# Kernel tuning notes

Measured on AMD Instinct MI355X. Metric: run time of the kernel, lower is better.

Reference implementation:

```python
import jax, jax.numpy as jnp
import numpy as np

T = 2_000_000  # timesteps


def setup_inputs() -> dict:
    key = jax.random.key(0)
    u = jax.random.normal(key, (T, 2), dtype=jnp.float32) * 10.0  # external forces per step
    x0 = jnp.zeros((4,), dtype=jnp.float32)  # [z1, v1, z2, v2]
    c = jnp.array([10.0, 10.0, 10.0], dtype=jnp.float32)   # trainable damping c1,c2,c3
    m = jnp.array([20.0, 10.0], dtype=jnp.float32)          # masses m1,m2 (frozen)
    k = jnp.array([2.0e3, 1.0e3, 5.0e3], dtype=jnp.float32) # stiffness k1,k2,k3 (frozen)
    dt = jnp.float32(0.002)
    return {"u": u, "x0": x0, "c": c, "m": m, "k": k, "dt": dt}


def reference(u, x0, c, m, k, dt):
    c1, c2, c3 = c[0], c[1], c[2]
    m1, m2 = m[0], m[1]
    k1, k2, k3 = k[0], k[1], k[2]

    def deriv(x, ut):
        # x = [z1, v1, z2, v2]; returns dx/dt = [v1, a1, v2, a2]
        z1, v1, z2, v2 = x[0], x[1], x[2], x[3]
        a1 = (ut[0] - (c1 + c2) * v1 + c2 * v2 - (k1 + k2) * z1 + k2 * z2) / m1
        a2 = (ut[1] - (c3 + c2) * v2 + c2 * v1 - (k3 + k2) * z2 + k2 * z1) / m2
        return jnp.stack([v1, a1, v2, a2])

    half = dt * 0.5

    def step(x, ut):
        s1 = deriv(x, ut)
        s2 = deriv(x + half * s1, ut)
        s3 = deriv(x + half * s2, ut)
        s4 = deriv(x + dt * s3, ut)
        xn = x + (dt / 6.0) * (s1 + 2.0 * s2 + 2.0 * s3 + s4)
        y = jnp.stack([xn[0], xn[2]])  # positions z1, z2 (matches cell output)
        return xn, y

    _, ys = jax.lax.scan(step, x0, u)
    return ys  # [T, 2]
```

## Files before the change

### kernel.cpp

```cpp
#include <hip/hip_runtime.h>

#define BLK 256
#define LS  16
#define SPB (BLK*LS)
#define STR (LS+1)

#define WS_M   0
#define WS_N   16
#define WS_SK  24
#define WS_GK  152
#define WS_AGG 304
#define WS_S1  2352

#define STEP4(Mx,Nx, s0,s1,s2,s3, ux,uy, n0,n1,n2,n3)                                              \
  n0 = fmaf(Mx[0],s0,  fmaf(Mx[1],s1,  fmaf(Mx[2],s2,  fmaf(Mx[3],s3,  fmaf(Nx[0],ux, Nx[1]*uy))))); \
  n1 = fmaf(Mx[4],s0,  fmaf(Mx[5],s1,  fmaf(Mx[6],s2,  fmaf(Mx[7],s3,  fmaf(Nx[2],ux, Nx[3]*uy))))); \
  n2 = fmaf(Mx[8],s0,  fmaf(Mx[9],s1,  fmaf(Mx[10],s2, fmaf(Mx[11],s3, fmaf(Nx[4],ux, Nx[5]*uy))))); \
  n3 = fmaf(Mx[12],s0, fmaf(Mx[13],s1, fmaf(Mx[14],s2, fmaf(Mx[15],s3, fmaf(Nx[6],ux, Nx[7]*uy)))));

__device__ __forceinline__ float4 aff_apply(const float* Mx, float4 l, float4 c) {
  float4 r;
  r.x = fmaf(Mx[0],l.x,  fmaf(Mx[1],l.y,  fmaf(Mx[2],l.z,  fmaf(Mx[3],l.w,  c.x))));
  r.y = fmaf(Mx[4],l.x,  fmaf(Mx[5],l.y,  fmaf(Mx[6],l.z,  fmaf(Mx[7],l.w,  c.y))));
  r.z = fmaf(Mx[8],l.x,  fmaf(Mx[9],l.y,  fmaf(Mx[10],l.z, fmaf(Mx[11],l.w, c.z))));
  r.w = fmaf(Mx[12],l.x, fmaf(Mx[13],l.y, fmaf(Mx[14],l.z, fmaf(Mx[15],l.w, c.w))));
  return r;
}

__device__ __forceinline__ float4 matvec(const float* Mx, float4 v) {
  return aff_apply(Mx, v, make_float4(0.f, 0.f, 0.f, 0.f));
}

__device__ __forceinline__ void mm4d(const double* X, const double* Y, double* Z) {
  for (int i = 0; i < 4; ++i)
    for (int j = 0; j < 4; ++j) {
      double s = 0.0;
      for (int l = 0; l < 4; ++l) s += X[i*4+l] * Y[l*4+j];
      Z[i*4+j] = s;
    }
}

__global__ void k_setup(const float* __restrict__ cin, const float* __restrict__ min_,
                        const float* __restrict__ kin, const float* __restrict__ dtin,
                        float* __restrict__ ws) {
  double c1 = cin[0], c2 = cin[1], c3 = cin[2];
  double m1 = min_[0], m2 = min_[1];
  double k1 = kin[0], k2 = kin[1], k3 = kin[2];
  double h  = dtin[0];

  double A[16] = { 0.0, 1.0, 0.0, 0.0,
                  -(k1+k2)/m1, -(c1+c2)/m1,  k2/m1,  c2/m1,
                   0.0, 0.0, 0.0, 1.0,
                   k2/m2,  c2/m2, -(k3+k2)/m2, -(c3+c2)/m2 };

  double Q[16], R[16], S[16], M[16], tmp[16];
  for (int i = 0; i < 16; ++i) Q[i] = ((i % 5 == 0) ? 1.0 : 0.0) + (h/4.0)*A[i];
  mm4d(A, Q, tmp);
  for (int i = 0; i < 16; ++i) R[i] = ((i % 5 == 0) ? 1.0 : 0.0) + (h/3.0)*tmp[i];
  mm4d(A, R, tmp);
  for (int i = 0; i < 16; ++i) S[i] = ((i % 5 == 0) ? 1.0 : 0.0) + (h/2.0)*tmp[i];
  mm4d(A, S, tmp);
  for (int i = 0; i < 16; ++i) M[i] = ((i % 5 == 0) ? 1.0 : 0.0) + h*tmp[i];

  double N[8];
  for (int i = 0; i < 4; ++i) {
    N[2*i+0] = h * S[i*4+1] / m1;
    N[2*i+1] = h * S[i*4+3] / m2;
  }

  for (int i = 0; i < 16; ++i) ws[WS_M+i] = (float)M[i];
  for (int i = 0; i < 8;  ++i) ws[WS_N+i] = (float)N[i];

  double P[16]; for (int i = 0; i < 16; ++i) P[i] = M[i];
  for (int r = 0; r < 4; ++r) { mm4d(P, P, tmp); for (int i = 0; i < 16; ++i) P[i] = tmp[i]; }

  for (int i = 0; i < 16; ++i) ws[WS_SK+i] = (float)P[i];
  for (int k = 1; k < 8; ++k) {
    mm4d(P, P, tmp); for (int i = 0; i < 16; ++i) P[i] = tmp[i];
    for (int i = 0; i < 16; ++i) ws[WS_SK+16*k+i] = (float)P[i];
  }
  mm4d(P, P, tmp); for (int i = 0; i < 16; ++i) P[i] = tmp[i];
  for (int i = 0; i < 16; ++i) ws[WS_GK+i] = (float)P[i];
  for (int k = 1; k < 9; ++k) {
    mm4d(P, P, tmp); for (int i = 0; i < 16; ++i) P[i] = tmp[i];
    for (int i = 0; i < 16; ++i) ws[WS_GK+16*k+i] = (float)P[i];
  }
}

__launch_bounds__(BLK)
__global__ void k_pass1(const float4* __restrict__ u4, const float* __restrict__ ws,
                        float4* __restrict__ s1out, float4* __restrict__ agg, int T2) {
  __shared__ float  uxp[BLK*STR];
  __shared__ float  uyp[BLK*STR];
  __shared__ float4 S1[BLK];
  __shared__ float  SKs[8*16];
  const int tid   = threadIdx.x;
  const int bid   = blockIdx.x;
  const int base2 = bid * SPB;

  float Mm[16], Nn[8];
  #pragma unroll
  for (int i = 0; i < 16; ++i) Mm[i] = ws[WS_M+i];
  #pragma unroll
  for (int i = 0; i < 8;  ++i) Nn[i] = ws[WS_N+i];
  if (tid < 128) SKs[tid] = ws[WS_SK + tid];

  #pragma unroll
  for (int kk = 0; kk < SPB/2/BLK; ++kk) {
    int idx4 = tid + kk*BLK;
    int s0 = 2*idx4;
    float4 v = make_float4(0.f, 0.f, 0.f, 0.f);
    if (base2 + s0 < T2) v = u4[(base2 >> 1) + idx4];
    int t0 = s0 >> 4, j0 = s0 & 15;
    int t1 = (s0+1) >> 4, j1 = (s0+1) & 15;
    uxp[t0*STR + j0] = v.x;  uyp[t0*STR + j0] = v.y;
    uxp[t1*STR + j1] = v.z;  uyp[t1*STR + j1] = v.w;
  }
  __syncthreads();

  float b0 = 0.f, b1 = 0.f, b2 = 0.f, b3 = 0.f;
  #pragma unroll
  for (int j = 0; j < LS; ++j) {
    float ux = uxp[tid*STR + j], uy = uyp[tid*STR + j];
    float n0, n1, n2, n3;
    STEP4(Mm, Nn, b0, b1, b2, b3, ux, uy, n0, n1, n2, n3);
    b0 = n0; b1 = n1; b2 = n2; b3 = n3;
  }
  S1[tid] = make_float4(b0, b1, b2, b3);
  __syncthreads();

  #pragma unroll
  for (int k = 0; k < 8; ++k) {
    int off = 1 << k;
    float4 l, c;
    bool act = (tid >= off);
    if (act) { l = S1[tid - off]; c = S1[tid]; }
    __syncthreads();
    if (act) S1[tid] = aff_apply(&SKs[16*k], l, c);
    __syncthreads();
  }

  s1out[bid * BLK + tid] = S1[tid];
  if (tid == BLK-1) agg[bid] = S1[BLK-1];
}

__launch_bounds__(BLK)
__global__ void k_pass3(const float4* __restrict__ u4, const float* __restrict__ ws,
                        const float4* __restrict__ s1buf, const float4* __restrict__ agg,
                        const float* __restrict__ x0in, float4* __restrict__ out4,
                        int T2, int nblk) {
  __shared__ float  uxp[BLK*STR];
  __shared__ float  uyp[BLK*STR];
  __shared__ float4 MA[512];
  __shared__ float4 MB[512];
  __shared__ float  SKs[8*16];
  __shared__ float  GKs[9*16];
  const int tid   = threadIdx.x;
  const int bid   = blockIdx.x;
  const int base2 = bid * SPB;

  float Mm[16], Nn[8];
  #pragma unroll
  for (int i = 0; i < 16; ++i) Mm[i] = ws[WS_M+i];
  #pragma unroll
  for (int i = 0; i < 8;  ++i) Nn[i] = ws[WS_N+i];
  if (tid < 128) SKs[tid] = ws[WS_SK + tid];
  if (tid < 144) GKs[tid] = ws[WS_GK + tid];

  #pragma unroll
  for (int kk = 0; kk < SPB/2/BLK; ++kk) {
    int idx4 = tid + kk*BLK;
    int s0 = 2*idx4;
    float4 v = make_float4(0.f, 0.f, 0.f, 0.f);
    if (base2 + s0 < T2) v = u4[(base2 >> 1) + idx4];
    int t0 = s0 >> 4, j0 = s0 & 15;
    int t1 = (s0+1) >> 4, j1 = (s0+1) & 15;
    uxp[t0*STR + j0] = v.x;  uyp[t0*STR + j0] = v.y;
    uxp[t1*STR + j1] = v.z;  uyp[t1*STR + j1] = v.w;
  }

  const int n = nblk + 1;
  #pragma unroll
  for (int j = 0; j < 2; ++j) {
    int i = tid + BLK*j;
    if (i < n) MA[i] = (i == 0) ? make_float4(x0in[0], x0in[1], x0in[2], x0in[3])
                                : agg[i-1];
  }
  __syncthreads();

  float4* Aa = MA; float4* Bb = MB;
  for (int k = 0; k < 9; ++k) {
    int off = 1 << k;
    if (off >= n) break;
    #pragma unroll
    for (int j = 0; j < 2; ++j) {
      int i = tid + BLK*j;
      if (i < n) {
        float4 v = Aa[i];
        if (i >= off) v = aff_apply(&GKs[16*k], Aa[i-off], v);
        Bb[i] = v;
      }
    }
    __syncthreads();
    float4* t = Aa; Aa = Bb; Bb = t;
  }

  float4 Xbs = Aa[bid];

  float4 v = Xbs;
  #pragma unroll
  for (int k = 0; k < 8; ++k)
    if (tid & (1 << k)) v = matvec(&SKs[16*k], v);
  float4 p = (tid > 0) ? s1buf[bid*BLK + tid - 1] : make_float4(0.f, 0.f, 0.f, 0.f);
  float x0 = v.x + p.x, x1 = v.y + p.y, x2 = v.z + p.z, x3 = v.w + p.w;

  #pragma unroll
  for (int j = 0; j < LS; ++j) {
    float ux = uxp[tid*STR + j], uy = uyp[tid*STR + j];
    float n0, n1, n2, n3;
    STEP4(Mm, Nn, x0, x1, x2, x3, ux, uy, n0, n1, n2, n3);
    x0 = n0; x1 = n1; x2 = n2; x3 = n3;
    uxp[tid*STR + j] = x0;
    uyp[tid*STR + j] = x2;
  }
  __syncthreads();

  #pragma unroll
  for (int kk = 0; kk < SPB/2/BLK; ++kk) {
    int idx4 = tid + kk*BLK;
    int s0 = 2*idx4;
    if (base2 + s0 < T2) {
      int t0 = s0 >> 4, j0 = s0 & 15;
      int t1 = (s0+1) >> 4, j1 = (s0+1) & 15;
      out4[(base2 >> 1) + idx4] = make_float4(uxp[t0*STR + j0], uyp[t0*STR + j0],
                                              uxp[t1*STR + j1], uyp[t1*STR + j1]);
    }
  }
}

extern "C" void kernel_launch(void* const* d_in, const int* in_sizes, int n_in,
                              void* d_out, int out_size, void* d_ws, size_t ws_size,
                              hipStream_t stream) {
  const float* u   = (const float*)d_in[0];
  const float* x0  = (const float*)d_in[1];
  const float* cc  = (const float*)d_in[2];
  const float* mm  = (const float*)d_in[3];
  const float* kk  = (const float*)d_in[4];
  const float* dt  = (const float*)d_in[5];

  const int T2   = in_sizes[0] / 2;
  const int nblk = (T2 + SPB - 1) / SPB;

  float*  ws   = (float*)d_ws;
  float4* agg  = (float4*)(ws + WS_AGG);
  float4* s1b  = (float4*)(ws + WS_S1);

  k_setup<<<1, 1, 0, stream>>>(cc, mm, kk, dt, ws);
  k_pass1<<<nblk, BLK, 0, stream>>>((const float4*)u, ws, s1b, agg, T2);
  k_pass3<<<nblk, BLK, 0, stream>>>((const float4*)u, ws, s1b, agg, x0,
                                    (float4*)d_out, T2, nblk);
}
```

Before: 98.51 us.

## Fuse serial setup kernel into pass kernels via wave-parallel shuffle matmuls

Removes the single-thread k_setup launch and instead has the first wavefront of every block in both passes compute the RK4 propagator, input matrix and power tables redundantly. It uses one lane per matrix element and __shfl in double precision. This eliminates a serial single-lane kernel and one launch on the critical path, along with the global-memory round trip for the coefficients. In exchange every block pays a few dozen shuffle-based double matmuls, though that work overlaps with its input loads.

```diff
diff --git a/kernel.cpp b/kernel.cpp
--- a/kernel.cpp
+++ b/kernel.cpp
@@ -5,12 +5,8 @@
 #define SPB (BLK*LS)
 #define STR (LS+1)
 
-#define WS_M   0
-#define WS_N   16
-#define WS_SK  24
-#define WS_GK  152
-#define WS_AGG 304
-#define WS_S1  2352
+#define WS_AGG 0
+#define WS_S1  2048
 
 #define STEP4(Mx,Nx, s0,s1,s2,s3, ux,uy, n0,n1,n2,n3)                                              \
   n0 = fmaf(Mx[0],s0,  fmaf(Mx[1],s1,  fmaf(Mx[2],s2,  fmaf(Mx[3],s3,  fmaf(Nx[0],ux, Nx[1]*uy))))); \
@@ -31,79 +27,85 @@
   return aff_apply(Mx, v, make_float4(0.f, 0.f, 0.f, 0.f));
 }
 
-__device__ __forceinline__ void mm4d(const double* X, const double* Y, double* Z) {
-  for (int i = 0; i < 4; ++i)
-    for (int j = 0; j < 4; ++j) {
-      double s = 0.0;
-      for (int l = 0; l < 4; ++l) s += X[i*4+l] * Y[l*4+j];
-      Z[i*4+j] = s;
-    }
-}
-
-__global__ void k_setup(const float* __restrict__ cin, const float* __restrict__ min_,
-                        const float* __restrict__ kin, const float* __restrict__ dtin,
-                        float* __restrict__ ws) {
+__device__ __forceinline__ double mm_el(double x, double y, int i, int j) {
+  double s = 0.0;
+  #pragma unroll
+  for (int l = 0; l < 4; ++l)
+    s = fma(__shfl(x, 4*i + l, 64), __shfl(y, 4*l + j, 64), s);
+  return s;
+}
+
+__device__ __forceinline__ void wave_setup(const float* __restrict__ cin,
+                                           const float* __restrict__ min_,
+                                           const float* __restrict__ kin,
+                                           const float* __restrict__ dtin,
+                                           float* Ms, float* Ns, float* SKs, float* GKs,
+                                           int lane, bool wantGK) {
   double c1 = cin[0], c2 = cin[1], c3 = cin[2];
   double m1 = min_[0], m2 = min_[1];
   double k1 = kin[0], k2 = kin[1], k3 = kin[2];
   double h  = dtin[0];
-
-  double A[16] = { 0.0, 1.0, 0.0, 0.0,
-                  -(k1+k2)/m1, -(c1+c2)/m1,  k2/m1,  c2/m1,
-                   0.0, 0.0, 0.0, 1.0,
-                   k2/m2,  c2/m2, -(k3+k2)/m2, -(c3+c2)/m2 };
-
-  double Q[16], R[16], S[16], M[16], tmp[16];
-  for (int i = 0; i < 16; ++i) Q[i] = ((i % 5 == 0) ? 1.0 : 0.0) + (h/4.0)*A[i];
-  mm4d(A, Q, tmp);
-  for (int i = 0; i < 16; ++i) R[i] = ((i % 5 == 0) ? 1.0 : 0.0) + (h/3.0)*tmp[i];
-  mm4d(A, R, tmp);
-  for (int i = 0; i < 16; ++i) S[i] = ((i % 5 == 0) ? 1.0 : 0.0) + (h/2.0)*tmp[i];
-  mm4d(A, S, tmp);
-  for (int i = 0; i < 16; ++i) M[i] = ((i % 5 == 0) ? 1.0 : 0.0) + h*tmp[i];
-
-  double N[8];
-  for (int i = 0; i < 4; ++i) {
-    N[2*i+0] = h * S[i*4+1] / m1;
-    N[2*i+1] = h * S[i*4+3] / m2;
-  }
-
-  for (int i = 0; i < 16; ++i) ws[WS_M+i] = (float)M[i];
-  for (int i = 0; i < 8;  ++i) ws[WS_N+i] = (float)N[i];
-
-  double P[16]; for (int i = 0; i < 16; ++i) P[i] = M[i];
-  for (int r = 0; r < 4; ++r) { mm4d(P, P, tmp); for (int i = 0; i < 16; ++i) P[i] = tmp[i]; }
-
-  for (int i = 0; i < 16; ++i) ws[WS_SK+i] = (float)P[i];
+  const int i = (lane >> 2) & 3, j = lane & 3;
+
+  double a;
+  if (i == 0)      a = (j == 1) ? 1.0 : 0.0;
+  else if (i == 2) a = (j == 3) ? 1.0 : 0.0;
+  else if (i == 1) a = (j==0) ? -(k1+k2)/m1 : (j==1) ? -(c1+c2)/m1
+                     : (j==2) ?  k2/m1      :  c2/m1;
+  else             a = (j==0) ?  k2/m2      : (j==1) ?  c2/m2
+                     : (j==2) ? -(k3+k2)/m2 : -(c3+c2)/m2;
+
+  const double id = (i == j) ? 1.0 : 0.0;
+  double q  = id + (h/4.0)*a;
+  double t  = mm_el(a, q,  i, j);
+  double r  = id + (h/3.0)*t;
+  t         = mm_el(a, r,  i, j);
+  double s_ = id + (h/2.0)*t;
+  t         = mm_el(a, s_, i, j);
+  double m  = id + h*t;
+  if (lane < 16) Ms[lane] = (float)m;
+
+  {
+    int e = lane & 7, ii = e >> 1, jp = e & 1, col = jp ? 3 : 1;
+    double sv = __shfl(s_, 4*ii + col, 64);
+    double nv = h * sv / (jp ? m2 : m1);
+    if (lane < 8) Ns[lane] = (float)nv;
+  }
+
+  double p = m;
+  #pragma unroll
+  for (int rr = 0; rr < 4; ++rr) p = mm_el(p, p, i, j);
+  if (lane < 16) SKs[lane] = (float)p;
+  #pragma unroll
   for (int k = 1; k < 8; ++k) {
-    mm4d(P, P, tmp); for (int i = 0; i < 16; ++i) P[i] = tmp[i];
-    for (int i = 0; i < 16; ++i) ws[WS_SK+16*k+i] = (float)P[i];
-  }
-  mm4d(P, P, tmp); for (int i = 0; i < 16; ++i) P[i] = tmp[i];
-  for (int i = 0; i < 16; ++i) ws[WS_GK+i] = (float)P[i];
-  for (int k = 1; k < 9; ++k) {
-    mm4d(P, P, tmp); for (int i = 0; i < 16; ++i) P[i] = tmp[i];
-    for (int i = 0; i < 16; ++i) ws[WS_GK+16*k+i] = (float)P[i];
+    p = mm_el(p, p, i, j);
+    if (lane < 16) SKs[16*k + lane] = (float)p;
+  }
+  if (wantGK) {
+    p = mm_el(p, p, i, j);
+    if (lane < 16) GKs[lane] = (float)p;
+    #pragma unroll
+    for (int k = 1; k < 9; ++k) {
+      p = mm_el(p, p, i, j);
+      if (lane < 16) GKs[16*k + lane] = (float)p;
+    }
   }
 }
 
 __launch_bounds__(BLK)
-__global__ void k_pass1(const float4* __restrict__ u4, const float* __restrict__ ws,
+__global__ void k_pass1(const float4* __restrict__ u4,
+                        const float* __restrict__ cc, const float* __restrict__ mmp,
+                        const float* __restrict__ kp, const float* __restrict__ dtp,
                         float4* __restrict__ s1out, float4* __restrict__ agg, int T2) {
   __shared__ float  uxp[BLK*STR];
   __shared__ float  uyp[BLK*STR];
   __shared__ float4 S1[BLK];
-  __shared__ float  SKs[8*16];
+  __shared__ float  Ms[16], Ns[8], SKs[8*16];
   const int tid   = threadIdx.x;
   const int bid   = blockIdx.x;
   const int base2 = bid * SPB;
 
-  float Mm[16], Nn[8];
-  #pragma unroll
-  for (int i = 0; i < 16; ++i) Mm[i] = ws[WS_M+i];
-  #pragma unroll
-  for (int i = 0; i < 8;  ++i) Nn[i] = ws[WS_N+i];
-  if (tid < 128) SKs[tid] = ws[WS_SK + tid];
+  if (tid < 64) wave_setup(cc, mmp, kp, dtp, Ms, Ns, SKs, nullptr, tid, false);
 
   #pragma unroll
   for (int kk = 0; kk < SPB/2/BLK; ++kk) {
@@ -118,6 +120,12 @@
   }
   __syncthreads();
 
+  float Mm[16], Nn[8];
+  #pragma unroll
+  for (int i = 0; i < 16; ++i) Mm[i] = Ms[i];
+  #pragma unroll
+  for (int i = 0; i < 8;  ++i) Nn[i] = Ns[i];
+
   float b0 = 0.f, b1 = 0.f, b2 = 0.f, b3 = 0.f;
   #pragma unroll
   for (int j = 0; j < LS; ++j) {
@@ -145,7 +153,9 @@
 }
 
 __launch_bounds__(BLK)
-__global__ void k_pass3(const float4* __restrict__ u4, const float* __restrict__ ws,
+__global__ void k_pass3(const float4* __restrict__ u4,
+                        const float* __restrict__ cc, const float* __restrict__ mmp,
+                        const float* __restrict__ kp, const float* __restrict__ dtp,
                         const float4* __restrict__ s1buf, const float4* __restrict__ agg,
                         const float* __restrict__ x0in, float4* __restrict__ out4,
                         int T2, int nblk) {
@@ -153,19 +163,12 @@
   __shared__ float  uyp[BLK*STR];
   __shared__ float4 MA[512];
   __shared__ float4 MB[512];
-  __shared__ float  SKs[8*16];
-  __shared__ float  GKs[9*16];
+  __shared__ float  Ms[16], Ns[8], SKs[8*16], GKs[9*16];
   const int tid   = threadIdx.x;
   const int bid   = blockIdx.x;
   const int base2 = bid * SPB;
 
-  float Mm[16], Nn[8];
-  #pragma unroll
-  for (int i = 0; i < 16; ++i) Mm[i] = ws[WS_M+i];
-  #pragma unroll
-  for (int i = 0; i < 8;  ++i) Nn[i] = ws[WS_N+i];
-  if (tid < 128) SKs[tid] = ws[WS_SK + tid];
-  if (tid < 144) GKs[tid] = ws[WS_GK + tid];
+  if (tid < 64) wave_setup(cc, mmp, kp, dtp, Ms, Ns, SKs, GKs, tid, true);
 
   #pragma unroll
   for (int kk = 0; kk < SPB/2/BLK; ++kk) {
@@ -187,6 +190,12 @@
                                 : agg[i-1];
   }
   __syncthreads();
+
+  float Mm[16], Nn[8];
+  #pragma unroll
+  for (int i = 0; i < 16; ++i) Mm[i] = Ms[i];
+  #pragma unroll
+  for (int i = 0; i < 8;  ++i) Nn[i] = Ns[i];
 
   float4* Aa = MA; float4* Bb = MB;
   for (int k = 0; k < 9; ++k) {
@@ -251,12 +260,11 @@
   const int T2   = in_sizes[0] / 2;
   const int nblk = (T2 + SPB - 1) / SPB;
 
-  float*  ws   = (float*)d_ws;
-  float4* agg  = (float4*)(ws + WS_AGG);
-  float4* s1b  = (float4*)(ws + WS_S1);
-
-  k_setup<<<1, 1, 0, stream>>>(cc, mm, kk, dt, ws);
-  k_pass1<<<nblk, BLK, 0, stream>>>((const float4*)u, ws, s1b, agg, T2);
-  k_pass3<<<nblk, BLK, 0, stream>>>((const float4*)u, ws, s1b, agg, x0,
+  float*  ws  = (float*)d_ws;
+  float4* agg = (float4*)(ws + WS_AGG);
+  float4* s1b = (float4*)(ws + WS_S1);
+
+  k_pass1<<<nblk, BLK, 0, stream>>>((const float4*)u, cc, mm, kk, dt, s1b, agg, T2);
+  k_pass3<<<nblk, BLK, 0, stream>>>((const float4*)u, cc, mm, kk, dt, s1b, agg, x0,
                                     (float4*)d_out, T2, nblk);
 }
```

Result: faster. 95.32 us (-3.2%).
